# Kernel tuning notes

Hardware: AMD Instinct MI355X
Metric: run time of the kernel (lower is better)

The kernel has to match this reference:

```python
import jax, jax.numpy as jnp
import numpy as np

B, N, C, H = 4, 2048, 1024, 16
D = C // H
SCALE = D ** -0.5


def setup_inputs() -> dict:
    key = jax.random.key(0)
    k1, k2, k3 = jax.random.split(key, 3)
    x = jax.random.normal(k1, (B, N, C), dtype=jnp.float32)
    w_qkv = jax.random.normal(k2, (C, 3 * C), dtype=jnp.float32) * (C ** -0.5)
    w_proj = jax.random.normal(k3, (C, C), dtype=jnp.float32) * (C ** -0.5)
    b_proj = jnp.zeros((C,), dtype=jnp.float32)
    return {"x": x, "w_qkv": w_qkv, "w_proj": w_proj, "b_proj": b_proj}


def reference(x, w_qkv, w_proj, b_proj):
    # qkv projection (no bias): [B,N,3C] -> [3,B,H,N,D]
    qkv = (x @ w_qkv).reshape(B, N, 3, H, D).transpose(2, 0, 3, 1, 4)
    q, k, v = qkv[0], qkv[1], qkv[2]
    # scores [B,H,N,N]
    attn = jax.nn.softmax(jnp.einsum('bhnd,bhmd->bhnm', q, k) * SCALE, axis=-1)
    out = jnp.einsum('bhnm,bhmd->bhnd', attn, v)          # [B,H,N,D]
    out = out.transpose(0, 2, 1, 3).reshape(B, N, C)       # [B,N,C]
    return out @ w_proj + b_proj
```

## Files before the change

kernel.cpp:

```cpp
#include <hip/hip_runtime.h>
#include <hip/hip_bf16.h>
#include <cstdint>
#include <cstddef>

typedef unsigned int uint;
typedef unsigned short ushort;

constexpr int Bn = 4, Nn = 2048, Cc = 1024, Hh = 16;
constexpr int ROWS = Bn * Nn;
constexpr int QKVC = 3 * Cc;
constexpr float SL2 = 0.18033688011118f;

typedef __bf16 bf16_t;
typedef bf16_t bf16x8 __attribute__((ext_vector_type(8)));
typedef float f32x4 __attribute__((ext_vector_type(4)));

__device__ __forceinline__ ushort f2bf(float f) {
  union { __bf16 b; ushort u; } cv;
  cv.b = (__bf16)f;
  return cv.u;
}
__device__ __forceinline__ float exp2v(float x) { return __builtin_exp2f(x); }

__device__ __forceinline__ void gload_lds16(const void* g, void* l) {
  __builtin_amdgcn_global_load_lds(
      (const __attribute__((address_space(1))) void*)g,
      (__attribute__((address_space(3))) void*)l, 16, 0, 0);
}

__global__ __launch_bounds__(256) void cvt_bf16_kernel(
    const float* __restrict__ in, ushort* __restrict__ out) {
  int i = blockIdx.x * 256 + threadIdx.x;
  const float4* ip = (const float4*)in;
  float4 a = ip[i * 2], b = ip[i * 2 + 1];
  uint4 w;
  w.x = (uint)f2bf(a.x) | ((uint)f2bf(a.y) << 16);
  w.y = (uint)f2bf(a.z) | ((uint)f2bf(a.w) << 16);
  w.z = (uint)f2bf(b.x) | ((uint)f2bf(b.y) << 16);
  w.w = (uint)f2bf(b.z) | ((uint)f2bf(b.w) << 16);
  ((uint4*)out)[i] = w;
}

__global__ __launch_bounds__(256) void transpose_cvt_kernel(
    const float* __restrict__ W, ushort* __restrict__ Wt, int K, int N) {
  __shared__ float tile[64][65];
  const int n0 = blockIdx.x * 64, k0 = blockIdx.y * 64;
  const int tid = threadIdx.x;
#pragma unroll
  for (int it = 0; it < 16; it++) {
    int idx = tid + it * 256;
    int r = idx >> 6, c = idx & 63;
    tile[r][c] = W[(size_t)(k0 + r) * N + n0 + c];
  }
  __syncthreads();
#pragma unroll
  for (int it = 0; it < 16; it++) {
    int idx = tid + it * 256;
    int r = idx >> 6, c = idx & 63;
    Wt[(size_t)(n0 + r) * K + k0 + c] = f2bf(tile[c][r]);
  }
}

template <int MODE>
__global__ __launch_bounds__(256) void gemm128_kernel(
    const ushort* __restrict__ A, const ushort* __restrict__ Bt,
    void* __restrict__ Cout, void* __restrict__ Vout,
    const float* __restrict__ bias, int M, int N, int K) {
  __shared__ ushort As[128 * 32];
  __shared__ ushort Bs[128 * 32];
  const int tid = threadIdx.x;
  const int lane = tid & 63;
  const int wid = tid >> 6;
  const int wm = wid >> 1, wn = wid & 1;
  const int l16 = lane & 15, g = lane >> 4;
  const int n0 = blockIdx.x * 128, m0 = blockIdx.y * 128;

  const int c0 = tid, c1 = tid + 256;
  const ushort* Ab = A + (size_t)m0 * K;
  const ushort* Bb = Bt + (size_t)n0 * K;
  f32x4 acc[4][4] = {};

  for (int k0 = 0; k0 < K; k0 += 32) {
    gload_lds16(Ab + (size_t)(c0 >> 2) * K + k0 + (c0 & 3) * 8, As + c0 * 8);
    gload_lds16(Ab + (size_t)(c1 >> 2) * K + k0 + (c1 & 3) * 8, As + c1 * 8);
    gload_lds16(Bb + (size_t)(c0 >> 2) * K + k0 + (c0 & 3) * 8, Bs + c0 * 8);
    gload_lds16(Bb + (size_t)(c1 >> 2) * K + k0 + (c1 & 3) * 8, Bs + c1 * 8);
    __syncthreads();
    bf16x8 af[4], bfr[4];
#pragma unroll
    for (int mf = 0; mf < 4; mf++)
      af[mf] = *(const bf16x8*)(As + (wm * 64 + mf * 16 + l16) * 32 + g * 8);
#pragma unroll
    for (int nf = 0; nf < 4; nf++)
      bfr[nf] = *(const bf16x8*)(Bs + (wn * 64 + nf * 16 + l16) * 32 + g * 8);
#pragma unroll
    for (int mf = 0; mf < 4; mf++)
#pragma unroll
      for (int nf = 0; nf < 4; nf++)
        acc[mf][nf] = __builtin_amdgcn_mfma_f32_16x16x32_bf16(af[mf], bfr[nf], acc[mf][nf], 0, 0, 0);
    __syncthreads();
  }

#pragma unroll
  for (int mf = 0; mf < 4; mf++) {
    const int orow0 = m0 + wm * 64 + mf * 16 + g * 4;
#pragma unroll
    for (int nf = 0; nf < 4; nf++) {
      int col = n0 + wn * 64 + nf * 16 + l16;
      if (MODE == 0) {
        if (col < 2048) {
          const float qs = (col < 1024) ? SL2 : 1.0f;
#pragma unroll
          for (int r = 0; r < 4; r++)
            ((ushort*)Cout)[(size_t)(orow0 + r) * 2048 + col] = f2bf(acc[mf][nf][r] * qs);
        } else {
          int hh = (col - 2048) >> 6, dd = (col - 2048) & 63;
          int bb = orow0 >> 11, nn = orow0 & 2047;
          ushort4 w;
          w.x = f2bf(acc[mf][nf][0]); w.y = f2bf(acc[mf][nf][1]);
          w.z = f2bf(acc[mf][nf][2]); w.w = f2bf(acc[mf][nf][3]);
          *(ushort4*)((ushort*)Vout + ((size_t)(bb * 16 + hh) * 64 + dd) * 2048 + nn) = w;
        }
      } else {
#pragma unroll
        for (int r = 0; r < 4; r++)
          ((float*)Cout)[(size_t)(orow0 + r) * N + col] = acc[mf][nf][r] + bias[col];
      }
    }
  }
}

__global__ __launch_bounds__(256, 4) void flash_mfma_kernel(
    const ushort* __restrict__ qk, const ushort* __restrict__ vt,
    ushort* __restrict__ obf) {
  __shared__ ushort Ks[2][64 * 64];
  __shared__ ushort Vs[2][64 * 64];
  const int tid = threadIdx.x;
  const int lane = tid & 63, wid = tid >> 6;
  const int l16 = lane & 15, g = lane >> 4;

  const int f = blockIdx.x + (int)(gridDim.x * blockIdx.y);
  const int xcd = f & 7, slot = f >> 3;
  const int bh = xcd * 8 + (slot >> 4);
  const int qx = slot & 15;
  const int b = bh >> 4, h = bh & 15;
  const int q0 = qx * 128 + wid * 32;

  const int sc0 = tid, sc1 = tid + 256;
  const int sr0 = sc0 >> 3, scol0 = ((sc0 & 7) ^ (sr0 & 7)) * 8;
  const int sr1 = sc1 >> 3, scol1 = ((sc1 & 7) ^ (sr1 & 7)) * 8;
  const ushort* Kbase = qk + (size_t)b * Nn * 2048 + 1024 + h * 64;
  const ushort* Vbase = vt + (size_t)bh * 64 * 2048;

#define STAGE(buf, kv0)                                                       \
  do {                                                                        \
    gload_lds16(Kbase + (size_t)((kv0) + sr0) * 2048 + scol0,                 \
                &Ks[buf][0] + sc0 * 8);                                       \
    gload_lds16(Kbase + (size_t)((kv0) + sr1) * 2048 + scol1,                 \
                &Ks[buf][0] + sc1 * 8);                                       \
    gload_lds16(Vbase + (size_t)sr0 * 2048 + (kv0) + scol0,                   \
                &Vs[buf][0] + sc0 * 8);                                       \
    gload_lds16(Vbase + (size_t)sr1 * 2048 + (kv0) + scol1,                   \
                &Vs[buf][0] + sc1 * 8);                                       \
  } while (0)

  bf16x8 qf[2][2];
#pragma unroll
  for (int qh = 0; qh < 2; qh++)
#pragma unroll
    for (int kc = 0; kc < 2; kc++)
      qf[qh][kc] = *(const bf16x8*)(
          qk + (size_t)(b * Nn + q0 + qh * 16 + l16) * 2048 + h * 64 + kc * 32 + g * 8);

  union { ushort us[8]; bf16x8 v; } onesu;
#pragma unroll
  for (int j = 0; j < 8; j++) onesu.us[j] = 0x3F80;
  const bf16x8 ones = onesu.v;

  f32x4 oacc[2][4] = {};
  f32x4 lacc[2] = {};

  STAGE(0, 0);

  for (int t = 0; t < Nn / 64; ++t) {
    const int cur = t & 1;
    asm volatile("s_waitcnt vmcnt(0)" ::: "memory");
    __builtin_amdgcn_s_barrier();
    asm volatile("" ::: "memory");
    if (t < Nn / 64 - 1) STAGE(cur ^ 1, (t + 1) * 64);

    const ushort* Kc = &Ks[cur][0];
    const ushort* Vc = &Vs[cur][0];

    f32x4 sacc[2][4] = {};
    __builtin_amdgcn_s_setprio(1);
#pragma unroll
    for (int kc = 0; kc < 2; kc++) {
#pragma unroll
      for (int jc = 0; jc < 4; jc++) {
        int row = jc * 16 + l16;
        bf16x8 kf = *(const bf16x8*)(Kc + row * 64 + ((kc * 32 + g * 8) ^ ((row & 7) << 3)));
        sacc[0][jc] = __builtin_amdgcn_mfma_f32_16x16x32_bf16(kf, qf[0][kc], sacc[0][jc], 0, 0, 0);
        sacc[1][jc] = __builtin_amdgcn_mfma_f32_16x16x32_bf16(kf, qf[1][kc], sacc[1][jc], 0, 0, 0);
      }
    }
    __builtin_amdgcn_s_setprio(0);

    bf16x8 pa[2][2];
#pragma unroll
    for (int qh = 0; qh < 2; qh++) {
      uint pk_[4][2];
#pragma unroll
      for (int jc = 0; jc < 4; jc++) {
        float p0 = exp2v(sacc[qh][jc][0]);
        float p1 = exp2v(sacc[qh][jc][1]);
        float p2 = exp2v(sacc[qh][jc][2]);
        float p3 = exp2v(sacc[qh][jc][3]);
        asm("v_cvt_pk_bf16_f32 %0, %1, %2" : "=v"(pk_[jc][0]) : "v"(p0), "v"(p1));
        asm("v_cvt_pk_bf16_f32 %0, %1, %2" : "=v"(pk_[jc][1]) : "v"(p2), "v"(p3));
      }
#pragma unroll
      for (int kc = 0; kc < 2; kc++) {
        uint a0 = pk_[kc * 2][0], b0 = pk_[kc * 2 + 1][0];
        asm("v_permlane32_swap_b32 %0, %1" : "+v"(a0), "+v"(b0));
        asm("v_permlane16_swap_b32 %0, %1" : "+v"(a0), "+v"(b0));
        uint a1 = pk_[kc * 2][1], b1 = pk_[kc * 2 + 1][1];
        asm("v_permlane32_swap_b32 %0, %1" : "+v"(a1), "+v"(b1));
        asm("v_permlane16_swap_b32 %0, %1" : "+v"(a1), "+v"(b1));
        union { uint4 u; bf16x8 v; } cv;
        cv.u.x = a0; cv.u.y = a1; cv.u.z = b0; cv.u.w = b1;
        pa[qh][kc] = cv.v;
      }
    }

    __builtin_amdgcn_s_setprio(1);
#pragma unroll
    for (int kc = 0; kc < 2; kc++) {
#pragma unroll
      for (int dc = 0; dc < 4; dc++) {
        int row = dc * 16 + l16;
        bf16x8 vf = *(const bf16x8*)(Vc + row * 64 + ((kc * 32 + g * 8) ^ ((row & 7) << 3)));
        oacc[0][dc] = __builtin_amdgcn_mfma_f32_16x16x32_bf16(pa[0][kc], vf, oacc[0][dc], 0, 0, 0);
        oacc[1][dc] = __builtin_amdgcn_mfma_f32_16x16x32_bf16(pa[1][kc], vf, oacc[1][dc], 0, 0, 0);
      }
      lacc[0] = __builtin_amdgcn_mfma_f32_16x16x32_bf16(pa[0][kc], ones, lacc[0], 0, 0, 0);
      lacc[1] = __builtin_amdgcn_mfma_f32_16x16x32_bf16(pa[1][kc], ones, lacc[1], 0, 0, 0);
    }
    __builtin_amdgcn_s_setprio(0);
  }
#undef STAGE

#pragma unroll
  for (int qh = 0; qh < 2; qh++) {
    f32x4 linv;
#pragma unroll
    for (int r = 0; r < 4; r++) linv[r] = 1.f / lacc[qh][r];
#pragma unroll
    for (int r = 0; r < 4; r++) {
      int grow = b * Nn + q0 + qh * 16 + g * 4 + r;
      ushort* op = obf + (size_t)grow * Cc + h * 64 + l16;
#pragma unroll
      for (int dc = 0; dc < 4; dc++)
        op[dc * 16] = f2bf(oacc[qh][dc][r] * linv[r]);
    }
  }
}

extern "C" void kernel_launch(void* const* d_in, const int* in_sizes, int n_in,
                              void* d_out, int out_size, void* d_ws, size_t ws_size,
                              hipStream_t stream) {
  const float* x      = (const float*)d_in[0];
  const float* w_qkv  = (const float*)d_in[1];
  const float* w_proj = (const float*)d_in[2];
  const float* b_proj = (const float*)d_in[3];
  float* out = (float*)d_out;

  char* ws = (char*)d_ws;
  ushort* Xbf    = (ushort*)(ws);
  ushort* WqkvT  = (ushort*)(ws + (16u << 20));
  ushort* WprojT = (ushort*)(ws + (22u << 20));
  ushort* QKbf   = (ushort*)(ws + (24u << 20));
  ushort* Vtg    = (ushort*)(ws + (56u << 20));
  ushort* Obf    = (ushort*)(ws + (72u << 20));

  cvt_bf16_kernel<<<4096, 256, 0, stream>>>(x, Xbf);
  transpose_cvt_kernel<<<dim3(QKVC / 64, Cc / 64), 256, 0, stream>>>(w_qkv, WqkvT, Cc, QKVC);
  transpose_cvt_kernel<<<dim3(Cc / 64, Cc / 64), 256, 0, stream>>>(w_proj, WprojT, Cc, Cc);
  gemm128_kernel<0><<<dim3(QKVC / 128, ROWS / 128), 256, 0, stream>>>(
      Xbf, WqkvT, QKbf, Vtg, nullptr, ROWS, QKVC, Cc);
  flash_mfma_kernel<<<dim3(Nn / 128, Bn * Hh), 256, 0, stream>>>(QKbf, Vtg, Obf);
  gemm128_kernel<1><<<dim3(Cc / 128, ROWS / 128), 256, 0, stream>>>(
      Obf, WprojT, out, nullptr, b_proj, ROWS, Cc, Cc);
}
```

Before: 227.2 us.

## Split attention KV range in two and merge partial outputs in a separate kernel

```diff
diff --git a/kernel.cpp b/kernel.cpp
--- a/kernel.cpp
+++ b/kernel.cpp
@@ -19,6 +19,11 @@
   union { __bf16 b; ushort u; } cv;
   cv.b = (__bf16)f;
   return cv.u;
+}
+__device__ __forceinline__ float bf2f(ushort u) {
+  union { float f; uint u; } cv;
+  cv.u = (uint)u << 16;
+  return cv.f;
 }
 __device__ __forceinline__ float exp2v(float x) { return __builtin_exp2f(x); }
 
@@ -130,9 +135,9 @@
   }
 }
 
-__global__ __launch_bounds__(256, 4) void flash_mfma_kernel(
+__global__ __launch_bounds__(256, 5) void flash_mfma_kernel(
     const ushort* __restrict__ qk, const ushort* __restrict__ vt,
-    ushort* __restrict__ obf) {
+    ushort* __restrict__ opart, float* __restrict__ lpart) {
   __shared__ ushort Ks[2][64 * 64];
   __shared__ ushort Vs[2][64 * 64];
   const int tid = threadIdx.x;
@@ -141,10 +146,13 @@
 
   const int f = blockIdx.x + (int)(gridDim.x * blockIdx.y);
   const int xcd = f & 7, slot = f >> 3;
-  const int bh = xcd * 8 + (slot >> 4);
-  const int qx = slot & 15;
+  const int bh = xcd * 8 + (slot >> 5);
+  const int w32 = slot & 31;
+  const int split = w32 >> 4;
+  const int qx = w32 & 15;
   const int b = bh >> 4, h = bh & 15;
   const int q0 = qx * 128 + wid * 32;
+  const int kvbase = split * (Nn / 2);
 
   const int sc0 = tid, sc1 = tid + 256;
   const int sr0 = sc0 >> 3, scol0 = ((sc0 & 7) ^ (sr0 & 7)) * 8;
@@ -180,14 +188,15 @@
   f32x4 oacc[2][4] = {};
   f32x4 lacc[2] = {};
 
-  STAGE(0, 0);
-
-  for (int t = 0; t < Nn / 64; ++t) {
+  STAGE(0, kvbase);
+
+  constexpr int NT = Nn / 2 / 64;
+  for (int t = 0; t < NT; ++t) {
     const int cur = t & 1;
     asm volatile("s_waitcnt vmcnt(0)" ::: "memory");
     __builtin_amdgcn_s_barrier();
     asm volatile("" ::: "memory");
-    if (t < Nn / 64 - 1) STAGE(cur ^ 1, (t + 1) * 64);
+    if (t < NT - 1) STAGE(cur ^ 1, kvbase + (t + 1) * 64);
 
     const ushort* Kc = &Ks[cur][0];
     const ushort* Vc = &Vs[cur][0];
@@ -250,20 +259,48 @@
   }
 #undef STAGE
 
+  ushort* ob = opart + (size_t)split * ROWS * Cc;
 #pragma unroll
   for (int qh = 0; qh < 2; qh++) {
-    f32x4 linv;
-#pragma unroll
-    for (int r = 0; r < 4; r++) linv[r] = 1.f / lacc[qh][r];
 #pragma unroll
     for (int r = 0; r < 4; r++) {
       int grow = b * Nn + q0 + qh * 16 + g * 4 + r;
-      ushort* op = obf + (size_t)grow * Cc + h * 64 + l16;
+      ushort* op = ob + (size_t)grow * Cc + h * 64 + l16;
 #pragma unroll
       for (int dc = 0; dc < 4; dc++)
-        op[dc * 16] = f2bf(oacc[qh][dc][r] * linv[r]);
-    }
-  }
+        op[dc * 16] = f2bf(oacc[qh][dc][r]);
+    }
+    if (l16 == 0) {
+#pragma unroll
+      for (int r = 0; r < 4; r++)
+        lpart[((size_t)split * 64 + bh) * Nn + (q0 + qh * 16 + g * 4 + r)] = lacc[qh][r];
+    }
+  }
+}
+
+__global__ __launch_bounds__(256) void merge_kernel(
+    const ushort* __restrict__ opart, const float* __restrict__ lpart,
+    ushort* __restrict__ out) {
+  int idx = blockIdx.x * 256 + threadIdx.x;
+  int row = idx >> 7;
+  int c8 = (idx & 127) << 3;
+  int b = row >> 11, q = row & 2047, h = c8 >> 6;
+  int bh = b * 16 + h;
+  float l0 = lpart[(size_t)bh * Nn + q];
+  float l1 = lpart[((size_t)64 + bh) * Nn + q];
+  float inv = 1.f / (l0 + l1);
+  const ushort* p0 = opart + (size_t)row * Cc + c8;
+  const ushort* p1 = p0 + (size_t)ROWS * Cc;
+  uint4 a = *(const uint4*)p0;
+  uint4 c = *(const uint4*)p1;
+  const ushort* au = (const ushort*)&a;
+  const ushort* cu = (const ushort*)&c;
+  uint4 w;
+  ushort* wu = (ushort*)&w;
+#pragma unroll
+  for (int j = 0; j < 8; j++)
+    wu[j] = f2bf((bf2f(au[j]) + bf2f(cu[j])) * inv);
+  *(uint4*)(out + (size_t)row * Cc + c8) = w;
 }
 
 extern "C" void kernel_launch(void* const* d_in, const int* in_sizes, int n_in,
@@ -281,14 +318,21 @@
   ushort* WprojT = (ushort*)(ws + (22u << 20));
   ushort* QKbf   = (ushort*)(ws + (24u << 20));
   ushort* Vtg    = (ushort*)(ws + (56u << 20));
-  ushort* Obf    = (ushort*)(ws + (72u << 20));
+  ushort* Opart  = (ushort*)(ws);
+  ushort* Opart1 = (ushort*)(ws + (72u << 20));
+  float*  Lpart  = (float*)(ws + (16u << 20));
+  ushort* Obf    = (ushort*)(ws + (56u << 20));
+  (void)Opart1;
+  Opart = (ushort*)(ws + (88u << 20));
+  Obf   = (ushort*)(ws);
 
   cvt_bf16_kernel<<<4096, 256, 0, stream>>>(x, Xbf);
   transpose_cvt_kernel<<<dim3(QKVC / 64, Cc / 64), 256, 0, stream>>>(w_qkv, WqkvT, Cc, QKVC);
   transpose_cvt_kernel<<<dim3(Cc / 64, Cc / 64), 256, 0, stream>>>(w_proj, WprojT, Cc, Cc);
   gemm128_kernel<0><<<dim3(QKVC / 128, ROWS / 128), 256, 0, stream>>>(
       Xbf, WqkvT, QKbf, Vtg, nullptr, ROWS, QKVC, Cc);
-  flash_mfma_kernel<<<dim3(Nn / 128, Bn * Hh), 256, 0, stream>>>(QKbf, Vtg, Obf);
+  flash_mfma_kernel<<<dim3(2 * Nn / 128, Bn * Hh), 256, 0, stream>>>(QKbf, Vtg, Opart, Lpart);
+  merge_kernel<<<4096, 256, 0, stream>>>(Opart, Lpart, Obf);
   gemm128_kernel<1><<<dim3(Cc / 128, ROWS / 128), 256, 0, stream>>>(
       Obf, WprojT, out, nullptr, b_proj, ROWS, Cc, Cc);
 }
```

After: 371.6 us. +63.5%, slower.

## Double GEMM K-tile to 64 and XOR-swizzle LDS layout

Applied to the files above, without the earlier changes.

```diff
diff --git a/kernel.cpp b/kernel.cpp
--- a/kernel.cpp
+++ b/kernel.cpp
@@ -66,8 +66,8 @@
     const ushort* __restrict__ A, const ushort* __restrict__ Bt,
     void* __restrict__ Cout, void* __restrict__ Vout,
     const float* __restrict__ bias, int M, int N, int K) {
-  __shared__ ushort As[128 * 32];
-  __shared__ ushort Bs[128 * 32];
+  __shared__ ushort As[128 * 64];
+  __shared__ ushort Bs[128 * 64];
   const int tid = threadIdx.x;
   const int lane = tid & 63;
   const int wid = tid >> 6;
@@ -75,29 +75,45 @@
   const int l16 = lane & 15, g = lane >> 4;
   const int n0 = blockIdx.x * 128, m0 = blockIdx.y * 128;
 
-  const int c0 = tid, c1 = tid + 256;
   const ushort* Ab = A + (size_t)m0 * K;
   const ushort* Bb = Bt + (size_t)n0 * K;
   f32x4 acc[4][4] = {};
 
-  for (int k0 = 0; k0 < K; k0 += 32) {
-    gload_lds16(Ab + (size_t)(c0 >> 2) * K + k0 + (c0 & 3) * 8, As + c0 * 8);
-    gload_lds16(Ab + (size_t)(c1 >> 2) * K + k0 + (c1 & 3) * 8, As + c1 * 8);
-    gload_lds16(Bb + (size_t)(c0 >> 2) * K + k0 + (c0 & 3) * 8, Bs + c0 * 8);
-    gload_lds16(Bb + (size_t)(c1 >> 2) * K + k0 + (c1 & 3) * 8, Bs + c1 * 8);
+  int srow[4], scol[4];
+#pragma unroll
+  for (int i = 0; i < 4; i++) {
+    int c = tid + i * 256;
+    srow[i] = c >> 3;
+    scol[i] = ((c & 7) ^ (srow[i] & 7)) * 8;
+  }
+
+  for (int k0 = 0; k0 < K; k0 += 64) {
+#pragma unroll
+    for (int i = 0; i < 4; i++) {
+      int c = tid + i * 256;
+      gload_lds16(Ab + (size_t)srow[i] * K + k0 + scol[i], As + c * 8);
+      gload_lds16(Bb + (size_t)srow[i] * K + k0 + scol[i], Bs + c * 8);
+    }
     __syncthreads();
-    bf16x8 af[4], bfr[4];
-#pragma unroll
-    for (int mf = 0; mf < 4; mf++)
-      af[mf] = *(const bf16x8*)(As + (wm * 64 + mf * 16 + l16) * 32 + g * 8);
-#pragma unroll
-    for (int nf = 0; nf < 4; nf++)
-      bfr[nf] = *(const bf16x8*)(Bs + (wn * 64 + nf * 16 + l16) * 32 + g * 8);
-#pragma unroll
-    for (int mf = 0; mf < 4; mf++)
-#pragma unroll
-      for (int nf = 0; nf < 4; nf++)
-        acc[mf][nf] = __builtin_amdgcn_mfma_f32_16x16x32_bf16(af[mf], bfr[nf], acc[mf][nf], 0, 0, 0);
+#pragma unroll
+    for (int kc = 0; kc < 2; kc++) {
+      bf16x8 af[4], bfr[4];
+#pragma unroll
+      for (int mf = 0; mf < 4; mf++) {
+        int row = wm * 64 + mf * 16 + l16;
+        af[mf] = *(const bf16x8*)(As + row * 64 + (((kc * 4 + g) ^ (row & 7)) * 8));
+      }
+#pragma unroll
+      for (int nf = 0; nf < 4; nf++) {
+        int row = wn * 64 + nf * 16 + l16;
+        bfr[nf] = *(const bf16x8*)(Bs + row * 64 + (((kc * 4 + g) ^ (row & 7)) * 8));
+      }
+#pragma unroll
+      for (int mf = 0; mf < 4; mf++)
+#pragma unroll
+        for (int nf = 0; nf < 4; nf++)
+          acc[mf][nf] = __builtin_amdgcn_mfma_f32_16x16x32_bf16(af[mf], bfr[nf], acc[mf][nf], 0, 0, 0);
+    }
     __syncthreads();
   }
 
```

New measurement: 209.0 us. 8.0% less time.
